# Optimization experiments

Measured on AMD Instinct MI355X. Metric: run time of the kernel, lower is better.

The kernel has to match this reference:

```python
import jax, jax.numpy as jnp
import numpy as np

B, A, C, M = 8, 98304, 80, 32
ALPHA, GAMMA = 0.25, 2.0


def setup_inputs() -> dict:
    key = jax.random.key(0)
    k1, k2, k3, k4, k5, k6, k7, k8 = jax.random.split(key, 8)
    classifications = jax.random.uniform(k1, (B, A, C), dtype=jnp.float32)
    regressions = jax.random.normal(k2, (B, A, 4), dtype=jnp.float32)
    # valid anchor boxes inside a 640px image
    ax = jax.random.uniform(k3, (A,)) * 512.0
    ay = jax.random.uniform(k4, (A,)) * 512.0
    aw = jax.random.uniform(k5, (A, 2)) * 120.0 + 8.0
    anchors = jnp.stack([ax, ay, ax + aw[:, 0], ay + aw[:, 1]], axis=-1)[None].astype(jnp.float32)
    # valid GT boxes with class labels in [0, C) (no -1 padding: all annotations valid)
    gx = jax.random.uniform(k6, (B, M, 2)) * 480.0
    gw = jax.random.uniform(k7, (B, M, 2)) * 150.0 + 10.0
    gcls = jax.random.randint(k8, (B, M), 0, C).astype(jnp.float32)
    annotations = jnp.concatenate([gx, gx + gw, gcls[..., None]], axis=-1).astype(jnp.float32)
    return {
        "classifications": classifications,
        "regressions": regressions,
        "anchors": anchors,
        "annotations": annotations,
        "negative_iou_thr": 0.4,
        "positive_iou_thr": 0.5,
    }


def calc_iou(a, b):
    # a: [A,4] anchors, b: [M,4] gt boxes -> [A,M]
    area = (b[:, 2] - b[:, 0]) * (b[:, 3] - b[:, 1])
    iw = jnp.clip(jnp.minimum(a[:, 2:3], b[:, 2]) - jnp.maximum(a[:, 0:1], b[:, 0]), 0.0)
    ih = jnp.clip(jnp.minimum(a[:, 3:4], b[:, 3]) - jnp.maximum(a[:, 1:2], b[:, 1]), 0.0)
    inter = iw * ih
    ua = jnp.clip(((a[:, 2] - a[:, 0]) * (a[:, 3] - a[:, 1]))[:, None] + area - inter, 1e-8)
    return inter / ua


def focal_loss(classifications, regressions, anchors, annotations, negative_iou_thr, positive_iou_thr):
    anchor = anchors[0]  # [A,4]
    aw = anchor[:, 2] - anchor[:, 0]
    ah = anchor[:, 3] - anchor[:, 1]
    acx = anchor[:, 0] + 0.5 * aw
    acy = anchor[:, 1] + 0.5 * ah

    def per_image(classification, regression, annot):
        p = jnp.clip(classification, 1e-4, 1.0 - 1e-4)
        valid = annot[:, 4] != -1.0  # [M] (all valid in test data)
        iou = jnp.where(valid[None, :], calc_iou(anchor, annot[:, :4]), -1.0)  # [A,M]
        iou_max = jnp.max(iou, axis=1)
        iou_arg = jnp.argmax(iou, axis=1)
        assigned = annot[iou_arg]  # [A,5]

        pos = iou_max >= positive_iou_thr  # [A]
        num_pos = jnp.sum(pos.astype(jnp.float32))
        onehot = jax.nn.one_hot(assigned[:, 4].astype(jnp.int32), C, dtype=jnp.float32)
        # targets: 1 for assigned class on positives, 0 elsewhere on pos/neg anchors, -1 ignored
        targets = jnp.where(pos[:, None], onehot,
                            jnp.where((iou_max < negative_iou_thr)[:, None], 0.0, -1.0))

        is_one = targets == 1.0
        alpha_factor = jnp.where(is_one, ALPHA, 1.0 - ALPHA)
        focal_w = alpha_factor * jnp.where(is_one, 1.0 - p, p) ** GAMMA
        bce = -(targets * jnp.log(p) + (1.0 - targets) * jnp.log(1.0 - p))
        cls_loss = jnp.where(targets != -1.0, focal_w * bce, 0.0)
        cls_loss = jnp.sum(cls_loss) / jnp.clip(num_pos, 1.0)

        gw = jnp.clip(assigned[:, 2] - assigned[:, 0], None, None)
        gh = assigned[:, 3] - assigned[:, 1]
        gcx = assigned[:, 0] + 0.5 * gw
        gcy = assigned[:, 1] + 0.5 * gh
        gw = jnp.clip(gw, 1.0)
        gh = jnp.clip(gh, 1.0)
        t = jnp.stack([(gcx - acx) / aw, (gcy - acy) / ah,
                       jnp.log(gw / aw), jnp.log(gh / ah)], axis=1)
        t = t / jnp.array([0.1, 0.1, 0.2, 0.2], dtype=jnp.float32)
        diff = jnp.abs(t - regression)
        sl1 = jnp.where(diff <= 1.0 / 9.0, 0.5 * 9.0 * diff * diff, diff - 0.5 / 9.0)
        reg_loss = jnp.sum(jnp.where(pos[:, None], sl1, 0.0)) / jnp.clip(num_pos * 4.0, 1.0)
        return cls_loss, reg_loss

    cls_l, reg_l = jax.vmap(per_image)(classifications, regressions, annotations)
    return jnp.mean(cls_l).reshape(1), jnp.mean(reg_l).reshape(1)


def reference(classifications, regressions, anchors, annotations, negative_iou_thr, positive_iou_thr):
    return focal_loss(classifications, regressions, anchors, annotations,
                      negative_iou_thr, positive_iou_thr)
```

## Files before the change

kernel.cpp:

```cpp
#include <hip/hip_runtime.h>

#define B_ 8
#define A_ 98304
#define C_ 80
#define M_ 32
#define BLK 256

#define NEGC (-0.75f * 0.69314718055994531f)

__device__ __forceinline__ float neg_u(float praw) {
    const float p = fminf(fmaxf(praw, 1e-4f), 1.0f - 1e-4f);
    return p * p * __log2f(1.0f - p);
}

__device__ __forceinline__ float smooth_l1(float t, float r) {
    float d = fabsf(t - r);
    return (d <= (1.0f / 9.0f)) ? (0.5f * 9.0f * d * d) : (d - 0.5f / 9.0f);
}

__global__ __launch_bounds__(BLK) void focal_main(
    const float* __restrict__ cls,
    const float* __restrict__ regr,
    const float* __restrict__ anchors,
    const float* __restrict__ ann,
    const float* __restrict__ neg_thr_p,
    const float* __restrict__ pos_thr_p,
    float* __restrict__ acc)
{
    __shared__ float s_x0[M_], s_y0[M_], s_x1[M_], s_y1[M_], s_ab[M_], s_cls[M_];
    __shared__ float s_w[BLK];
    __shared__ float s_red[(BLK / 64) * 3];

    const int tid = threadIdx.x;
    const int blocksPerImg = A_ / BLK;
    const int b  = blockIdx.x / blocksPerImg;
    const int a0 = (blockIdx.x % blocksPerImg) * BLK;

    if (tid < M_) {
        const float* am = ann + ((size_t)b * M_ + tid) * 5;
        const float x0 = am[0], y0 = am[1], x1 = am[2], y1 = am[3], cl = am[4];
        s_x0[tid] = x0; s_y0[tid] = y0; s_x1[tid] = x1; s_y1[tid] = y1;
        s_ab[tid] = (x1 - x0) * (y1 - y0);
        s_cls[tid] = cl;
    }
    __syncthreads();

    const float neg_thr = neg_thr_p[0];
    const float pos_thr = pos_thr_p[0];

    const int a = a0 + tid;
    const float4 an = reinterpret_cast<const float4*>(anchors)[a];
    const float aw = an.z - an.x;
    const float ah = an.w - an.y;
    const float areaA = aw * ah;

    float ib = -1.0f, ub = 1.0f;
    int   arg = 0;
#pragma unroll
    for (int m = 0; m < M_; ++m) {
        const float iw = fmaxf(fminf(an.z, s_x1[m]) - fmaxf(an.x, s_x0[m]), 0.0f);
        const float ih = fmaxf(fminf(an.w, s_y1[m]) - fmaxf(an.y, s_y0[m]), 0.0f);
        float inter = iw * ih;
        const float ua = fmaxf(areaA + s_ab[m] - inter, 1e-8f);
        if (s_cls[m] == -1.0f) inter = -1.0f;
        if (inter * ub > ib * ua) { ib = inter; ub = ua; arg = m; }
    }
    const bool pos = (ib >= pos_thr * ub);
    const bool neg = (ib <  neg_thr * ub);

    float reg_partial = 0.0f;
    float pos_count   = 0.0f;
    float cls_corr    = 0.0f;
    float cw = (pos || neg) ? NEGC : 0.0f;

    if (pos) {
        pos_count = 1.0f;
        const float gx0 = s_x0[arg], gy0 = s_y0[arg];
        const float gx1 = s_x1[arg], gy1 = s_y1[arg];
        const int   kcls = (int)s_cls[arg];

        float gw = gx1 - gx0;
        float gh = gy1 - gy0;
        const float gcx = gx0 + 0.5f * gw;
        const float gcy = gy0 + 0.5f * gh;
        gw = fmaxf(gw, 1.0f);
        gh = fmaxf(gh, 1.0f);
        const float acx = an.x + 0.5f * aw;
        const float acy = an.y + 0.5f * ah;
        const float t0 = ((gcx - acx) / aw) * 10.0f;
        const float t1 = ((gcy - acy) / ah) * 10.0f;
        const float t2 = logf(gw / aw) * 5.0f;
        const float t3 = logf(gh / ah) * 5.0f;
        const float4 r = reinterpret_cast<const float4*>(regr)[(size_t)b * A_ + a];
        reg_partial = smooth_l1(t0, r.x) + smooth_l1(t1, r.y) +
                      smooth_l1(t2, r.z) + smooth_l1(t3, r.w);

        const float praw = cls[((size_t)b * A_ + a) * C_ + kcls];
        const float p  = fminf(fmaxf(praw, 1e-4f), 1.0f - 1e-4f);
        const float om = 1.0f - p;
        const float negv = neg_u(praw) * NEGC;
        const float posv = 0.25f * om * om * (-__logf(p));
        cls_corr = posv - negv;
    }
    s_w[tid] = cw;
    __syncthreads();

    const float4* cls4 = reinterpret_cast<const float4*>(
        cls + ((size_t)b * A_ + a0) * C_);
    float cls_partial = cls_corr;
#pragma unroll 5
    for (int it = 0; it < (BLK * C_ / 4) / BLK; ++it) {
        const int vid = it * BLK + tid;
        const float4 v = cls4[vid];
        const int al = vid / 20;
        const float cw2 = s_w[al];
        const float u = (neg_u(v.x) + neg_u(v.y)) + (neg_u(v.z) + neg_u(v.w));
        cls_partial = fmaf(u, cw2, cls_partial);
    }

#pragma unroll
    for (int off = 32; off > 0; off >>= 1) {
        cls_partial += __shfl_down(cls_partial, off);
        reg_partial += __shfl_down(reg_partial, off);
        pos_count   += __shfl_down(pos_count,   off);
    }
    const int wave = tid >> 6;
    if ((tid & 63) == 0) {
        s_red[wave * 3 + 0] = cls_partial;
        s_red[wave * 3 + 1] = reg_partial;
        s_red[wave * 3 + 2] = pos_count;
    }
    __syncthreads();
    if (tid == 0) {
        float c = 0.0f, r = 0.0f, n = 0.0f;
#pragma unroll
        for (int w = 0; w < BLK / 64; ++w) {
            c += s_red[w * 3 + 0];
            r += s_red[w * 3 + 1];
            n += s_red[w * 3 + 2];
        }
        atomicAdd(&acc[b * 3 + 0], c);
        atomicAdd(&acc[b * 3 + 1], r);
        atomicAdd(&acc[b * 3 + 2], n);
    }
}

__global__ void focal_finalize(const float* __restrict__ acc, float* __restrict__ out) {
    const int t = threadIdx.x;
    float cls_l = 0.0f, reg_l = 0.0f;
    if (t < B_) {
        const float np = acc[t * 3 + 2];
        cls_l = acc[t * 3 + 0] / fmaxf(np, 1.0f);
        reg_l = acc[t * 3 + 1] / fmaxf(np * 4.0f, 1.0f);
    }
#pragma unroll
    for (int off = 32; off > 0; off >>= 1) {
        cls_l += __shfl_down(cls_l, off);
        reg_l += __shfl_down(reg_l, off);
    }
    if (t == 0) {
        out[0] = cls_l / (float)B_;
        out[1] = reg_l / (float)B_;
    }
}

extern "C" void kernel_launch(void* const* d_in, const int* in_sizes, int n_in,
                              void* d_out, int out_size, void* d_ws, size_t ws_size,
                              hipStream_t stream) {
    const float* cls     = (const float*)d_in[0];
    const float* regr    = (const float*)d_in[1];
    const float* anchors = (const float*)d_in[2];
    const float* ann     = (const float*)d_in[3];
    const float* negt    = (const float*)d_in[4];
    const float* post    = (const float*)d_in[5];
    float* acc = (float*)d_ws;

    hipMemsetAsync(acc, 0, B_ * 3 * sizeof(float), stream);
    focal_main<<<B_ * (A_ / BLK), BLK, 0, stream>>>(cls, regr, anchors, ann,
                                                    negt, post, acc);
    focal_finalize<<<1, 64, 0, stream>>>(acc, (float*)d_out);
}
```

Baseline: 117.5 us.

## Split focal loss into IoU-assignment kernel and streaming classification-sum kernel

Splits the fused kernel in two. The first kernel does anchor-to-GT matching, regression loss and the positive correction, and writes a per-anchor weight array to workspace. The second kernel streams the 252 MB classification tensor in larger per-block chunks, reading the weights back from global memory. The aim is to decouple the latency-bound IoU loop from the bandwidth-bound stream and to cut atomic traffic by skipping zero adds. The cost is an extra launch plus a small weight-array round trip through memory.

```diff
diff --git a/kernel.cpp b/kernel.cpp
--- a/kernel.cpp
+++ b/kernel.cpp
@@ -8,6 +8,11 @@
 
 #define NEGC (-0.75f * 0.69314718055994531f)
 
+#define P2_BLOCKS 256
+#define F4_PER_IMG (A_ * C_ / 4)
+#define F4_PER_BLK (F4_PER_IMG / P2_BLOCKS)
+#define P2_ITERS (F4_PER_BLK / BLK)
+
 __device__ __forceinline__ float neg_u(float praw) {
     const float p = fminf(fmaxf(praw, 1e-4f), 1.0f - 1e-4f);
     return p * p * __log2f(1.0f - p);
@@ -18,17 +23,17 @@
     return (d <= (1.0f / 9.0f)) ? (0.5f * 9.0f * d * d) : (d - 0.5f / 9.0f);
 }
 
-__global__ __launch_bounds__(BLK) void focal_main(
+__global__ __launch_bounds__(BLK) void focal_phase1(
     const float* __restrict__ cls,
     const float* __restrict__ regr,
     const float* __restrict__ anchors,
     const float* __restrict__ ann,
     const float* __restrict__ neg_thr_p,
     const float* __restrict__ pos_thr_p,
-    float* __restrict__ acc)
+    float* __restrict__ acc,
+    float* __restrict__ w)
 {
     __shared__ float s_x0[M_], s_y0[M_], s_x1[M_], s_y1[M_], s_ab[M_], s_cls[M_];
-    __shared__ float s_w[BLK];
     __shared__ float s_red[(BLK / 64) * 3];
 
     const int tid = threadIdx.x;
@@ -71,7 +76,6 @@
     float reg_partial = 0.0f;
     float pos_count   = 0.0f;
     float cls_corr    = 0.0f;
-    float cw = (pos || neg) ? NEGC : 0.0f;
 
     if (pos) {
         pos_count = 1.0f;
@@ -102,31 +106,17 @@
         const float posv = 0.25f * om * om * (-__logf(p));
         cls_corr = posv - negv;
     }
-    s_w[tid] = cw;
-    __syncthreads();
-
-    const float4* cls4 = reinterpret_cast<const float4*>(
-        cls + ((size_t)b * A_ + a0) * C_);
-    float cls_partial = cls_corr;
-#pragma unroll 5
-    for (int it = 0; it < (BLK * C_ / 4) / BLK; ++it) {
-        const int vid = it * BLK + tid;
-        const float4 v = cls4[vid];
-        const int al = vid / 20;
-        const float cw2 = s_w[al];
-        const float u = (neg_u(v.x) + neg_u(v.y)) + (neg_u(v.z) + neg_u(v.w));
-        cls_partial = fmaf(u, cw2, cls_partial);
-    }
+    w[(size_t)b * A_ + a] = (pos || neg) ? NEGC : 0.0f;
 
 #pragma unroll
     for (int off = 32; off > 0; off >>= 1) {
-        cls_partial += __shfl_down(cls_partial, off);
+        cls_corr    += __shfl_down(cls_corr,    off);
         reg_partial += __shfl_down(reg_partial, off);
         pos_count   += __shfl_down(pos_count,   off);
     }
     const int wave = tid >> 6;
     if ((tid & 63) == 0) {
-        s_red[wave * 3 + 0] = cls_partial;
+        s_red[wave * 3 + 0] = cls_corr;
         s_red[wave * 3 + 1] = reg_partial;
         s_red[wave * 3 + 2] = pos_count;
     }
@@ -134,14 +124,49 @@
     if (tid == 0) {
         float c = 0.0f, r = 0.0f, n = 0.0f;
 #pragma unroll
-        for (int w = 0; w < BLK / 64; ++w) {
-            c += s_red[w * 3 + 0];
-            r += s_red[w * 3 + 1];
-            n += s_red[w * 3 + 2];
+        for (int wv = 0; wv < BLK / 64; ++wv) {
+            c += s_red[wv * 3 + 0];
+            r += s_red[wv * 3 + 1];
+            n += s_red[wv * 3 + 2];
         }
-        atomicAdd(&acc[b * 3 + 0], c);
-        atomicAdd(&acc[b * 3 + 1], r);
-        atomicAdd(&acc[b * 3 + 2], n);
+        if (c != 0.0f) atomicAdd(&acc[b * 3 + 0], c);
+        if (r != 0.0f) atomicAdd(&acc[b * 3 + 1], r);
+        if (n != 0.0f) atomicAdd(&acc[b * 3 + 2], n);
+    }
+}
+
+__global__ __launch_bounds__(BLK) void focal_phase2(
+    const float4* __restrict__ cls4,
+    const float* __restrict__ w,
+    float* __restrict__ acc)
+{
+    const int tid = threadIdx.x;
+    const int b   = blockIdx.x / P2_BLOCKS;
+    const int blk = blockIdx.x % P2_BLOCKS;
+    const int lbase = blk * F4_PER_BLK;
+    const float4* img = cls4 + (size_t)b * F4_PER_IMG;
+    const float*  wb  = w + (size_t)b * A_;
+
+    float s = 0.0f;
+#pragma unroll 6
+    for (int it = 0; it < P2_ITERS; ++it) {
+        const int li = lbase + it * BLK + tid;
+        const float4 v = img[li];
+        const float cw = wb[(unsigned)li / 20u];
+        const float u = (neg_u(v.x) + neg_u(v.y)) + (neg_u(v.z) + neg_u(v.w));
+        s = fmaf(u, cw, s);
+    }
+
+#pragma unroll
+    for (int off = 32; off > 0; off >>= 1) s += __shfl_down(s, off);
+    __shared__ float red[BLK / 64];
+    if ((tid & 63) == 0) red[tid >> 6] = s;
+    __syncthreads();
+    if (tid == 0) {
+        float t = 0.0f;
+#pragma unroll
+        for (int i2 = 0; i2 < BLK / 64; ++i2) t += red[i2];
+        atomicAdd(&acc[b * 3 + 0], t);
     }
 }
 
@@ -173,10 +198,14 @@
     const float* ann     = (const float*)d_in[3];
     const float* negt    = (const float*)d_in[4];
     const float* post    = (const float*)d_in[5];
+
     float* acc = (float*)d_ws;
+    float* w   = (float*)d_ws + 64;
 
     hipMemsetAsync(acc, 0, B_ * 3 * sizeof(float), stream);
-    focal_main<<<B_ * (A_ / BLK), BLK, 0, stream>>>(cls, regr, anchors, ann,
-                                                    negt, post, acc);
+    focal_phase1<<<B_ * (A_ / BLK), BLK, 0, stream>>>(cls, regr, anchors, ann,
+                                                      negt, post, acc, w);
+    focal_phase2<<<B_ * P2_BLOCKS, BLK, 0, stream>>>(
+        reinterpret_cast<const float4*>(cls), w, acc);
     focal_finalize<<<1, 64, 0, stream>>>(acc, (float*)d_out);
 }
```

Measured after the change: 158.0 us. 34.5% more time.
